# Optimization experiments

Hardware: AMD Instinct MI355X
Metric: run time of the kernel (lower is better)

Reference implementation:

```python
import jax, jax.numpy as jnp
import numpy as np
from jax import lax

V, VE, DE, DX, HID, T, S = 100000, 1000, 256, 64, 512, 64, 2048
H = HID // 2


def setup_inputs() -> dict:
    key = jax.random.key(0)
    ks = jax.random.split(key, 18)
    def n(k, shape, scale=0.1):
        return jax.random.normal(k, shape, jnp.float32) * scale
    return {
        "sentence": jax.random.randint(ks[0], (S,), 0, V),
        "extra": jax.random.randint(ks[1], (S,), 0, VE),
        "b": 0,
        "e": S,
        "emb": n(ks[2], (V, DE)),
        "extra_emb": n(ks[3], (VE, DX)),
        "w_ih_f": n(ks[4], (4 * H, DE + DX)),
        "w_hh_f": n(ks[5], (4 * H, H)),
        "b_ih_f": n(ks[6], (4 * H,)),
        "b_hh_f": n(ks[7], (4 * H,)),
        "w_ih_b": n(ks[8], (4 * H, DE + DX)),
        "w_hh_b": n(ks[9], (4 * H, H)),
        "b_ih_b": n(ks[10], (4 * H,)),
        "b_hh_b": n(ks[11], (4 * H,)),
        "fc_w": n(ks[12], (T, HID)),
        "fc_b": n(ks[13], (T,)),
        "crf_start": n(ks[14], (T,)),
        "crf_end": n(ks[15], (T,)),
        "crf_trans": n(ks[16], (T, T)),
    }


def _lstm_dir(x, w_ih, w_hh, b_ih, b_hh):
    """Single-direction LSTM over x [S, D] with batch 1. PyTorch gate order i,f,g,o."""
    Hh = w_hh.shape[1]
    gx = x @ w_ih.T + (b_ih + b_hh)  # [S, 4H], input projection hoisted out of the scan

    def step(carry, g_in):
        h, c = carry
        g = g_in + h @ w_hh.T  # [4H]
        i, f, gg, o = jnp.split(g, 4)
        i = jax.nn.sigmoid(i)
        f = jax.nn.sigmoid(f)
        gg = jnp.tanh(gg)
        o = jax.nn.sigmoid(o)
        c = f * c + i * gg
        h = o * jnp.tanh(c)
        return (h, c), h

    init = (jnp.zeros((Hh,), x.dtype), jnp.zeros((Hh,), x.dtype))
    _, hs = lax.scan(step, init, gx)
    return hs  # [S, H]


def _lstm_feats(sentence, extra, emb, extra_emb,
                w_ih_f, w_hh_f, b_ih_f, b_hh_f,
                w_ih_b, w_hh_b, b_ih_b, b_hh_b, fc_w, fc_b):
    x = jnp.concatenate([emb[sentence], extra_emb[extra]], axis=1)  # [S, DE+DX]
    hf = _lstm_dir(x, w_ih_f, w_hh_f, b_ih_f, b_hh_f)              # [S, H]
    hb = _lstm_dir(x[::-1], w_ih_b, w_hh_b, b_ih_b, b_hh_b)[::-1]  # [S, H]
    lstm_out = jnp.concatenate([hf, hb], axis=1)                   # [S, 2H]
    return lstm_out @ fc_w.T + fc_b                                # [S, T]


def _viterbi_decode(feats, start, end, trans):
    """torchcrf-style Viterbi on feats [L, T]; returns best tag path [L] (int32)."""
    score0 = start + feats[0]  # [T]

    def step(score, emit_t):
        m = score[:, None] + trans + emit_t[None, :]  # [T_prev, T_next]
        return jnp.max(m, axis=0), jnp.argmax(m, axis=0).astype(jnp.int32)

    final_score, bps = lax.scan(step, score0, feats[1:])  # bps: [L-1, T]
    final_score = final_score + end
    last_tag = jnp.argmax(final_score).astype(jnp.int32)

    def back(tag, bp_t):
        prev = bp_t[tag]
        return prev, prev

    _, prev_tags = lax.scan(back, last_tag, bps[::-1])
    return jnp.concatenate([prev_tags[::-1], last_tag[None]])  # [L]


def reference(sentence, extra, b, e, emb, extra_emb,
              w_ih_f, w_hh_f, b_ih_f, b_hh_f,
              w_ih_b, w_hh_b, b_ih_b, b_hh_b,
              fc_w, fc_b, crf_start, crf_end, crf_trans):
    feats = _lstm_feats(sentence, extra, emb, extra_emb,
                        w_ih_f, w_hh_f, b_ih_f, b_hh_f,
                        w_ih_b, w_hh_b, b_ih_b, b_hh_b, fc_w, fc_b)
    feats = feats[b:e]  # static Python-int phrase bounds
    return _viterbi_decode(feats, crf_start, crf_end, crf_trans)
```

## Files before the change

### kernel.cpp

```cpp
#include <hip/hip_runtime.h>
#include <stdint.h>

#define SEQ   2048
#define DE    256
#define DXX   64
#define DIN   320
#define HH    256
#define G4    1024
#define NT    64

static constexpr size_t OFF_GX = 0;
static constexpr size_t OFF_H  = OFF_GX + (size_t)2 * SEQ * G4;
static constexpr size_t HSTR   = (size_t)SEQ * HH;
static constexpr size_t OFF_SL = OFF_H + 2 * HSTR;
static constexpr size_t OFF_FE = OFF_SL + 2048;
static constexpr size_t OFF_BP = OFF_FE + (size_t)SEQ * NT;
static constexpr size_t WS_NEEDED_BYTES = OFF_BP * 4 + (size_t)SEQ * NT;

__global__ __launch_bounds__(256) void k_init(unsigned long long* __restrict__ slot) {
  const int tid = threadIdx.x;
  #pragma unroll
  for (int b = 0; b < 4; ++b) slot[b * 256 + tid] = 0ull;
}

__global__ __launch_bounds__(512) void k_gx(
    const int* __restrict__ sent, const int* __restrict__ extra,
    const float* __restrict__ emb, const float* __restrict__ xemb,
    const float* __restrict__ wf, const float* __restrict__ wb,
    const float* __restrict__ bif, const float* __restrict__ bhf,
    const float* __restrict__ bib, const float* __restrict__ bhb,
    float* __restrict__ GX) {
  __shared__ __align__(16) float xs[32][36];
  __shared__ __align__(16) float wl[32][260];
  const int tid = threadIdx.x;
  const int s0 = blockIdx.x * 32, r0 = blockIdx.y * 256, dir = blockIdx.z;
  const float* W = dir ? wb : wf;
  const int tids = tid & 7;
  const int tidr = tid >> 3;
  float acc[4][4];
  #pragma unroll
  for (int a = 0; a < 4; ++a)
    #pragma unroll
    for (int b = 0; b < 4; ++b) acc[a][b] = 0.f;

  for (int kc = 0; kc < 10; ++kc) {
    const int k0 = kc * 32;
    __syncthreads();
    for (int e = tid; e < 1024; e += 512) {
      int kk = e & 31, sl = e >> 5;
      int s = s0 + sl;
      int src = dir ? (SEQ - 1 - s) : s;
      int k = k0 + kk;
      float v;
      if (k < DE) v = emb[(size_t)sent[src] * DE + k];
      else        v = xemb[(size_t)extra[src] * DXX + (k - DE)];
      xs[kk][sl] = v;
    }
    for (int e = tid; e < 8192; e += 512) {
      int kk = e & 31, rl = e >> 5;
      wl[kk][rl] = W[(size_t)(r0 + rl) * DIN + k0 + kk];
    }
    __syncthreads();
    #pragma unroll
    for (int kk = 0; kk < 32; ++kk) {
      float4 xv = *(const float4*)&xs[kk][4 * tids];
      float4 wv = *(const float4*)&wl[kk][4 * tidr];
      acc[0][0] += xv.x * wv.x; acc[0][1] += xv.x * wv.y; acc[0][2] += xv.x * wv.z; acc[0][3] += xv.x * wv.w;
      acc[1][0] += xv.y * wv.x; acc[1][1] += xv.y * wv.y; acc[1][2] += xv.y * wv.z; acc[1][3] += xv.y * wv.w;
      acc[2][0] += xv.z * wv.x; acc[2][1] += xv.z * wv.y; acc[2][2] += xv.z * wv.z; acc[2][3] += xv.z * wv.w;
      acc[3][0] += xv.w * wv.x; acc[3][1] += xv.w * wv.y; acc[3][2] += xv.w * wv.z; acc[3][3] += xv.w * wv.w;
    }
  }
  const float* BI = dir ? bib : bif;
  const float* BH = dir ? bhb : bhf;
  float4 b1 = *(const float4*)&BI[r0 + 4 * tidr];
  float4 b2 = *(const float4*)&BH[r0 + 4 * tidr];
  float bx = b1.x + b2.x, by = b1.y + b2.y, bz = b1.z + b2.z, bw = b1.w + b2.w;
  #pragma unroll
  for (int ss = 0; ss < 4; ++ss) {
    int s = s0 + 4 * tids + ss;
    float4 o;
    o.x = acc[ss][0] + bx; o.y = acc[ss][1] + by; o.z = acc[ss][2] + bz; o.w = acc[ss][3] + bw;
    *(float4*)&GX[((size_t)dir * SEQ + s) * G4 + r0 + 4 * tidr] = o;
  }
}

__global__ __launch_bounds__(256, 1) void k_lstm16(
    const float* __restrict__ whf, const float* __restrict__ whb,
    const float* __restrict__ GX, float* __restrict__ H,
    unsigned long long* __restrict__ slot) {
  const int dir = blockIdx.x >> 4;
  const int p   = blockIdx.x & 15;
  const int tid = threadIdx.x;
  const int rr  = tid >> 2;
  const int q   = tid & 3;
  const int gq  = rr >> 4;
  const int joq = rr & 15;
  const int rowQ = (gq << 8) | (p << 4) | joq;
  const int rowC = ((tid >> 4) << 8) | (p << 4) | (tid & 15);

  const float4* w4g =
      (const float4*)((dir ? whb : whf) + (size_t)rowQ * HH) + q * 16;
  float4 w[16];
  #pragma unroll
  for (int i = 0; i < 16; ++i) w[i] = w4g[i];
  #pragma unroll
  for (int i = 0; i < 16; ++i)
    asm volatile("" : "+v"(w[i].x), "+v"(w[i].y), "+v"(w[i].z), "+v"(w[i].w));

  const float* gxc = GX + (size_t)dir * SEQ * G4 + rowC;
  float* Hd = H + (size_t)dir * HSTR;
  unsigned long long* sl = slot + dir * 512;

  __shared__ __align__(16) float hl[HH];
  __shared__ float psum[256];
  __shared__ float gacc[64];
  float c = 0.f;
  int budget = 1 << 18;

  for (int t = 0; t < SEQ; ++t) {
    float gxv = 0.f;
    if (tid < 64) gxv = gxc[(size_t)t * G4];
    {
      unsigned long long* sp = &sl[(t & 1) * 256 + tid];
      unsigned long long v;
      do {
        v = __hip_atomic_load(sp, __ATOMIC_RELAXED, __HIP_MEMORY_SCOPE_AGENT);
      } while ((unsigned)(v >> 32) != (unsigned)t && --budget > 0);
      union { unsigned u; float f; } cv; cv.u = (unsigned)v;
      hl[tid] = cv.f;
    }
    __syncthreads();
    const float4* h4 = (const float4*)hl + q * 16;
    float a0 = 0.f, a1 = 0.f, a2 = 0.f, a3 = 0.f;
    #pragma unroll
    for (int i = 0; i < 16; ++i) {
      float4 wv = w[i];
      float4 hv = h4[i];
      a0 += wv.x * hv.x; a1 += wv.y * hv.y; a2 += wv.z * hv.z; a3 += wv.w * hv.w;
    }
    psum[tid] = (a0 + a1) + (a2 + a3);
    __syncthreads();
    if (tid < 64) {
      float s = gxv + ((psum[4 * tid] + psum[4 * tid + 1]) +
                       (psum[4 * tid + 2] + psum[4 * tid + 3]));
      gacc[tid] = s;
    }
    __syncthreads();
    if (tid < 16) {
      float iv = gacc[tid], fv = gacc[16 + tid], gv = gacc[32 + tid],
            ov = gacc[48 + tid];
      float ig = 1.f / (1.f + expf(-iv));
      float fg = 1.f / (1.f + expf(-fv));
      float gg = tanhf(gv);
      float og = 1.f / (1.f + expf(-ov));
      c = fg * c + ig * gg;
      float h = og * tanhf(c);
      int jj = (p << 4) | tid;
      Hd[(size_t)t * HH + jj] = h;
      union { float f; unsigned u; } hu; hu.f = h;
      unsigned long long pk =
          ((unsigned long long)(unsigned)(t + 1) << 32) | hu.u;
      __hip_atomic_store(&sl[((t + 1) & 1) * 256 + jj], pk, __ATOMIC_RELAXED,
                         __HIP_MEMORY_SCOPE_AGENT);
    }
  }
}

__global__ __launch_bounds__(256) void k_feats(
    const float* __restrict__ HF, const float* __restrict__ HB,
    const float* __restrict__ fcw, const float* __restrict__ fcb,
    float* __restrict__ FE) {
  __shared__ float hlds[16][512];
  __shared__ float wl[64][65];
  const int tid = threadIdx.x;
  const int s0 = blockIdx.x * 16;
  for (int e = tid; e < 16 * 512; e += 256) {
    int sl = e >> 9, k = e & 511;
    float v = (k < HH) ? HF[(size_t)(s0 + sl) * HH + k]
                       : HB[(size_t)(SEQ - 1 - (s0 + sl)) * HH + (k - HH)];
    hlds[sl][k] = v;
  }
  const int j = tid & 63, sg = tid >> 6;
  float acc[4];
  #pragma unroll
  for (int q = 0; q < 4; ++q) acc[q] = fcb[j];
  for (int kc = 0; kc < 8; ++kc) {
    __syncthreads();
    for (int e = tid; e < 4096; e += 256) {
      int kk = e & 63, jj = e >> 6;
      wl[kk][jj] = fcw[(size_t)jj * 512 + kc * 64 + kk];
    }
    __syncthreads();
    #pragma unroll 8
    for (int kk = 0; kk < 64; ++kk) {
      float wv = wl[kk][j];
      int kg = kc * 64 + kk;
      #pragma unroll
      for (int q = 0; q < 4; ++q) acc[q] += hlds[4 * sg + q][kg] * wv;
    }
  }
  #pragma unroll
  for (int q = 0; q < 4; ++q)
    FE[(size_t)(s0 + 4 * sg + q) * NT + j] = acc[q];
}

__global__ __launch_bounds__(256) void k_viterbi(
    const float* __restrict__ feats, const float* __restrict__ start,
    const float* __restrict__ endv, const float* __restrict__ trans,
    unsigned char* __restrict__ bp, int* __restrict__ out) {
  __shared__ float tr[64 * 64];
  __shared__ float sc[64];
  __shared__ float pval[4][64];
  __shared__ int pidx[4][64];
  const int tid = threadIdx.x;
  for (int e = tid; e < 4096; e += 256) tr[e] = trans[e];
  if (tid < 64) sc[tid] = start[tid] + feats[tid];
  __syncthreads();
  const int w = tid >> 6, j = tid & 63;
  for (int t = 1; t < SEQ; ++t) {
    float fj = feats[t * NT + j];
    float best = -3.0e38f; int bi = 0;
    const int ibase = w << 4;
    #pragma unroll
    for (int ii = 0; ii < 16; ++ii) {
      int i = ibase + ii;
      float v = (sc[i] + tr[(i << 6) | j]) + fj;
      if (v > best) { best = v; bi = i; }
    }
    pval[w][j] = best; pidx[w][j] = bi;
    __syncthreads();
    if (w == 0) {
      float b = pval[0][j]; int x = pidx[0][j];
      if (pval[1][j] > b) { b = pval[1][j]; x = pidx[1][j]; }
      if (pval[2][j] > b) { b = pval[2][j]; x = pidx[2][j]; }
      if (pval[3][j] > b) { b = pval[3][j]; x = pidx[3][j]; }
      bp[t * NT + j] = (unsigned char)x;
      sc[j] = b;
    }
    __syncthreads();
  }
  if (tid == 0) {
    float best = -3.0e38f; int bt = 0;
    for (int i = 0; i < 64; ++i) {
      float v = sc[i] + endv[i];
      if (v > best) { best = v; bt = i; }
    }
    out[SEQ - 1] = bt;
    int tag = bt;
    for (int t = SEQ - 1; t >= 1; --t) {
      tag = bp[t * NT + tag];
      out[t - 1] = tag;
    }
  }
}

extern "C" void kernel_launch(void* const* d_in, const int* in_sizes, int n_in,
                              void* d_out, int out_size, void* d_ws, size_t ws_size,
                              hipStream_t stream) {
  if (n_in < 19) return;
  if (in_sizes[0] != SEQ || in_sizes[1] != SEQ) return;
  if (in_sizes[2] != 1 || in_sizes[3] != 1) return;
  if (in_sizes[4] != 100000 * DE) return;
  if (in_sizes[5] != 1000 * DXX) return;
  if (in_sizes[6] != G4 * DIN || in_sizes[7] != G4 * HH) return;
  if (in_sizes[8] != G4 || in_sizes[9] != G4) return;
  if (in_sizes[10] != G4 * DIN || in_sizes[11] != G4 * HH) return;
  if (in_sizes[14] != NT * 512 || in_sizes[15] != NT) return;
  if (in_sizes[16] != NT || in_sizes[17] != NT) return;
  if (in_sizes[18] != NT * NT) return;
  if (out_size < SEQ) return;
  if (ws_size < WS_NEEDED_BYTES) return;

  const int*   sent = (const int*)d_in[0];
  const int*   extra = (const int*)d_in[1];
  const float* emb  = (const float*)d_in[4];
  const float* xemb = (const float*)d_in[5];
  const float* wihf = (const float*)d_in[6];
  const float* whhf = (const float*)d_in[7];
  const float* bihf = (const float*)d_in[8];
  const float* bhhf = (const float*)d_in[9];
  const float* wihb = (const float*)d_in[10];
  const float* whhb = (const float*)d_in[11];
  const float* bihb = (const float*)d_in[12];
  const float* bhhb = (const float*)d_in[13];
  const float* fcw  = (const float*)d_in[14];
  const float* fcb  = (const float*)d_in[15];
  const float* cst  = (const float*)d_in[16];
  const float* cen  = (const float*)d_in[17];
  const float* ctr  = (const float*)d_in[18];

  float* ws = (float*)d_ws;
  float* GX = ws + OFF_GX;
  float* H  = ws + OFF_H;
  unsigned long long* SLOT = (unsigned long long*)(ws + OFF_SL);
  float* FE = ws + OFF_FE;
  unsigned char* BP = (unsigned char*)(ws + OFF_BP);

  k_init<<<1, 256, 0, stream>>>(SLOT);
  k_gx<<<dim3(SEQ / 32, G4 / 256, 2), 512, 0, stream>>>(
      sent, extra, emb, xemb, wihf, wihb, bihf, bhhf, bihb, bhhb, GX);
  k_lstm16<<<32, 256, 0, stream>>>(whhf, whhb, GX, H, SLOT);
  k_feats<<<SEQ / 16, 256, 0, stream>>>(H, H + HSTR, fcw, fcb, FE);
  k_viterbi<<<1, 256, 0, stream>>>(FE, cst, cen, ctr, BP, (int*)d_out);
}
```

Baseline: 5.439 ms.

## Replace LDS reductions and extra barriers with wavefront shuffles in LSTM step

Remaps threads so that each group of 16 lanes holds the four gate rows and four K-quarter partials of one hidden unit. The partial-sum reduction and gate gathering then use wavefront shuffles instead of LDS arrays. This removes two __syncthreads per timestep from the serial recurrence. The h buffer is double-buffered by timestep and padded, so the single remaining barrier is enough. Each of the 16 hidden units is now finalized by one lane per 16-lane group, spread across waves, instead of all in the first 16 lanes.

```diff
diff --git a/kernel.cpp b/kernel.cpp
--- a/kernel.cpp
+++ b/kernel.cpp
@@ -92,15 +92,13 @@
   const int dir = blockIdx.x >> 4;
   const int p   = blockIdx.x & 15;
   const int tid = threadIdx.x;
-  const int rr  = tid >> 2;
   const int q   = tid & 3;
-  const int gq  = rr >> 4;
-  const int joq = rr & 15;
-  const int rowQ = (gq << 8) | (p << 4) | joq;
-  const int rowC = ((tid >> 4) << 8) | (p << 4) | (tid & 15);
+  const int g   = (tid >> 2) & 3;
+  const int j   = tid >> 4;
+  const int row = (g << 8) | (p << 4) | j;
 
   const float4* w4g =
-      (const float4*)((dir ? whb : whf) + (size_t)rowQ * HH) + q * 16;
+      (const float4*)((dir ? whb : whf) + (size_t)row * HH) + q * 16;
   float4 w[16];
   #pragma unroll
   for (int i = 0; i < 16; ++i) w[i] = w4g[i];
@@ -108,19 +106,19 @@
   for (int i = 0; i < 16; ++i)
     asm volatile("" : "+v"(w[i].x), "+v"(w[i].y), "+v"(w[i].z), "+v"(w[i].w));
 
-  const float* gxc = GX + (size_t)dir * SEQ * G4 + rowC;
+  const float* gxp = GX + (size_t)dir * SEQ * G4 + row;
   float* Hd = H + (size_t)dir * HSTR;
   unsigned long long* sl = slot + dir * 512;
 
-  __shared__ __align__(16) float hl[HH];
-  __shared__ float psum[256];
-  __shared__ float gacc[64];
+  __shared__ __align__(16) float hl[2][4][68];
   float c = 0.f;
   int budget = 1 << 18;
+  const int lane  = tid & 63;
+  const int lbase = lane & 48;
 
   for (int t = 0; t < SEQ; ++t) {
     float gxv = 0.f;
-    if (tid < 64) gxv = gxc[(size_t)t * G4];
+    if (q == 0) gxv = gxp[(size_t)t * G4];
     {
       unsigned long long* sp = &sl[(t & 1) * 256 + tid];
       unsigned long long v;
@@ -128,10 +126,10 @@
         v = __hip_atomic_load(sp, __ATOMIC_RELAXED, __HIP_MEMORY_SCOPE_AGENT);
       } while ((unsigned)(v >> 32) != (unsigned)t && --budget > 0);
       union { unsigned u; float f; } cv; cv.u = (unsigned)v;
-      hl[tid] = cv.f;
-    }
-    __syncthreads();
-    const float4* h4 = (const float4*)hl + q * 16;
+      hl[t & 1][tid >> 6][tid & 63] = cv.f;
+    }
+    __syncthreads();
+    const float4* h4 = (const float4*)hl[t & 1][q];
     float a0 = 0.f, a1 = 0.f, a2 = 0.f, a3 = 0.f;
     #pragma unroll
     for (int i = 0; i < 16; ++i) {
@@ -139,24 +137,21 @@
       float4 hv = h4[i];
       a0 += wv.x * hv.x; a1 += wv.y * hv.y; a2 += wv.z * hv.z; a3 += wv.w * hv.w;
     }
-    psum[tid] = (a0 + a1) + (a2 + a3);
-    __syncthreads();
-    if (tid < 64) {
-      float s = gxv + ((psum[4 * tid] + psum[4 * tid + 1]) +
-                       (psum[4 * tid + 2] + psum[4 * tid + 3]));
-      gacc[tid] = s;
-    }
-    __syncthreads();
-    if (tid < 16) {
-      float iv = gacc[tid], fv = gacc[16 + tid], gv = gacc[32 + tid],
-            ov = gacc[48 + tid];
-      float ig = 1.f / (1.f + expf(-iv));
-      float fg = 1.f / (1.f + expf(-fv));
-      float gg = tanhf(gv);
-      float og = 1.f / (1.f + expf(-ov));
+    float sr = (a0 + a1) + (a2 + a3);
+    sr += __shfl_xor(sr, 1);
+    sr += __shfl_xor(sr, 2);
+    float st = gxv + sr;
+    float s_f = __shfl(st, lbase + 4);
+    float s_g = __shfl(st, lbase + 8);
+    float s_o = __shfl(st, lbase + 12);
+    if ((tid & 15) == 0) {
+      float ig = 1.f / (1.f + expf(-st));
+      float fg = 1.f / (1.f + expf(-s_f));
+      float gg = tanhf(s_g);
+      float og = 1.f / (1.f + expf(-s_o));
       c = fg * c + ig * gg;
       float h = og * tanhf(c);
-      int jj = (p << 4) | tid;
+      int jj = (p << 4) | (tid >> 4);
       Hd[(size_t)t * HH + jj] = h;
       union { float f; unsigned u; } hu; hu.f = h;
       unsigned long long pk =
```

Result: slower. 6.334 ms (+16.4%).
